# Performance work log

Measured on AMD Instinct MI355X. Metric: run time of the kernel, lower is better.

Reference implementation:

```python
import jax, jax.numpy as jnp
import numpy as np
from jax import lax

B_, NF, H, W = 2, 8, 32, 32
DIM = 384            # mamba_feat_dim = pT*pH*pW*hid_dim = 2*2*2*48
D_INNER = 192        # expand=0.5 -> int(0.5*384)
D_STATE = 16
D_CONV = 4
DT_RANK = 24         # ceil(DIM/16)
HIDDEN = 1536        # mlp_ratio=4
L = NF * H * W


def _ln(x, w, b):
    m = x.mean(-1, keepdims=True)
    v = ((x - m) ** 2).mean(-1, keepdims=True)
    return (x - m) * lax.rsqrt(v + 1e-5) * w + b


def _mamba(xn, in_proj_w, conv_w, conv_b, xproj_w, dt_w, dt_b, A_log, Dp, out_proj_w):
    # xn: [b, L, DIM]
    b = xn.shape[0]
    xz = jnp.einsum('bld,ed->ble', xn, in_proj_w)            # [b,L,2*di]
    xp, z = xz[..., :D_INNER], xz[..., D_INNER:]
    # causal depthwise conv along L (mamba_ssm pads left d_conv-1)
    xc = lax.conv_general_dilated(xp.swapaxes(1, 2), conv_w[:, None, :], (1,),
                                  [(D_CONV - 1, 0)],
                                  dimension_numbers=('NCH', 'OIH', 'NCH'),
                                  feature_group_count=D_INNER) + conv_b[None, :, None]
    xc = jax.nn.silu(xc).swapaxes(1, 2)                      # [b,L,di]
    dbl = jnp.einsum('bld,ed->ble', xc, xproj_w)             # [b,L,dt_rank+2*ds]
    dt = jax.nn.softplus(jnp.einsum('blr,dr->bld', dbl[..., :DT_RANK], dt_w) + dt_b)
    Bm = dbl[..., DT_RANK:DT_RANK + D_STATE]
    Cm = dbl[..., DT_RANK + D_STATE:]
    A = -jnp.exp(A_log)                                      # [di,ds]

    def step(h, inp):
        dt_t, B_t, C_t, x_t = inp                            # [b,di],[b,ds],[b,ds],[b,di]
        dA = jnp.exp(dt_t[..., None] * A)                    # [b,di,ds]
        h = dA * h + dt_t[..., None] * B_t[:, None, :] * x_t[..., None]
        return h, jnp.einsum('bds,bs->bd', h, C_t)

    h0 = jnp.zeros((b, D_INNER, D_STATE), xn.dtype)
    _, ys = lax.scan(step, h0, (dt.swapaxes(0, 1), Bm.swapaxes(0, 1),
                                Cm.swapaxes(0, 1), xc.swapaxes(0, 1)))
    y = ys.swapaxes(0, 1) + Dp * xc
    y = y * jax.nn.silu(z)
    return jnp.einsum('ble,de->bld', y, out_proj_w)


def _ssa(seqs, ssa_w):
    # sequence shuffle attention: grouped 1x1 conv over per-sequence pooled features
    pooled = jnp.stack([s.mean(1) for s in seqs], 1)          # [b,3,c]
    w = jnp.einsum('bsd,dts->btd', pooled, ssa_w)             # per-channel 3x3 mix
    aw = jax.nn.softmax(w, axis=1)                            # softmax over sequences
    st = jnp.stack(seqs, 0)                                   # [3,b,L,c]
    return jnp.einsum('btd,tbld->bld', aw, st)


def _mlp(x, fc1_w, fc1_b, dw_w, dw_b, fc2_w, fc2_b):
    b = x.shape[0]
    h1 = jnp.einsum('bld,ed->ble', x, fc1_w) + fc1_b          # [b,L,HIDDEN]
    hv = h1.swapaxes(1, 2).reshape(b, HIDDEN, NF, H, W)
    hv = lax.conv_general_dilated(hv, dw_w, (1, 1, 1), [(1, 1)] * 3,
                                  dimension_numbers=('NCDHW', 'OIDHW', 'NCDHW'),
                                  feature_group_count=HIDDEN) + dw_b[None, :, None, None, None]
    h1 = hv.reshape(b, HIDDEN, L).swapaxes(1, 2)
    h1 = jax.nn.gelu(h1, approximate=False)
    return jnp.einsum('ble,de->bld', h1, fc2_w) + fc2_b


def _forward(x, freq_x, ln1_w, ln1_b, in_proj_w, conv_w, conv_b, xproj_w, dt_w, dt_b,
             A_log, Dp, out_proj_w, ssa_w, ln2_w, ln2_b, fc1_w, fc1_b, dw_w, dw_b,
             fc2_w, fc2_b, hilbert_curve):
    b = x.shape[0]
    xc = x.transpose(0, 2, 1, 3, 4).reshape(b, DIM, L)        # [b,c,L]
    x_flat = xc[:, :, hilbert_curve].swapaxes(1, 2)           # hilbert gather -> [b,L,c]
    fc = freq_x.transpose(0, 2, 1, 3, 4).reshape(b, DIM, L)
    f_flat = fc[:, :, hilbert_curve].swapaxes(1, 2)
    normed = _ln(x_flat, ln1_w, ln1_b)
    mparams = (in_proj_w, conv_w, conv_b, xproj_w, dt_w, dt_b, A_log, Dp, out_proj_w)
    m_fwd = _mamba(normed, *mparams)
    m_rev = jnp.flip(_mamba(jnp.flip(normed, 1), *mparams), 1)
    mo = _ssa([m_fwd, m_rev, f_flat], ssa_w)
    xm = x_flat + mo
    xm = xm + _mlp(_ln(xm, ln2_w, ln2_b), fc1_w, fc1_b, dw_w, dw_b, fc2_w, fc2_b)
    outm = xm.swapaxes(1, 2)                                  # [b,c,L]
    inv = jnp.argsort(hilbert_curve)                          # inverse permutation (scatter)
    uns = outm[:, :, inv]
    return uns.reshape(b, DIM, NF, H, W).transpose(0, 2, 1, 3, 4)


def setup_inputs() -> dict:
    key = jax.random.key(0)
    ks = jax.random.split(key, 12)
    def n(i, shape, s=0.02):
        return jax.random.normal(ks[i], shape, jnp.float32) * s
    perm = jnp.asarray(np.random.default_rng(0).permutation(L), jnp.int32)
    return {
        'x': jax.random.normal(ks[0], (B_, NF, DIM, H, W), jnp.float32),
        'freq_x': jax.random.normal(ks[1], (B_, NF, DIM, H, W), jnp.float32),
        'hilbert_curve': perm,
        'ln1_w': jnp.ones((DIM,), jnp.float32), 'ln1_b': jnp.zeros((DIM,), jnp.float32),
        'in_proj_w': n(2, (2 * D_INNER, DIM)),
        'conv_w': n(3, (D_INNER, D_CONV), 0.1), 'conv_b': jnp.zeros((D_INNER,), jnp.float32),
        'xproj_w': n(4, (DT_RANK + 2 * D_STATE, D_INNER)),
        'dt_w': n(5, (D_INNER, DT_RANK), 0.1),
        'dt_b': jnp.full((D_INNER,), -4.6, jnp.float32),
        'A_log': jnp.log(jnp.tile(jnp.arange(1, D_STATE + 1, dtype=jnp.float32)[None, :], (D_INNER, 1))),
        'Dp': jnp.ones((D_INNER,), jnp.float32),
        'out_proj_w': n(6, (DIM, D_INNER)),
        'ssa_w': n(7, (DIM, 3, 3)),
        'ln2_w': jnp.ones((DIM,), jnp.float32), 'ln2_b': jnp.zeros((DIM,), jnp.float32),
        'fc1_w': n(8, (HIDDEN, DIM)), 'fc1_b': jnp.zeros((HIDDEN,), jnp.float32),
        'dw_w': n(9, (HIDDEN, 1, 3, 3, 3), 0.05), 'dw_b': jnp.zeros((HIDDEN,), jnp.float32),
        'fc2_w': n(10, (DIM, HIDDEN)), 'fc2_b': jnp.zeros((DIM,), jnp.float32),
    }


def reference(x, freq_x, hilbert_curve, ln1_w, ln1_b, in_proj_w, conv_w, conv_b,
              xproj_w, dt_w, dt_b, A_log, Dp, out_proj_w, ssa_w, ln2_w, ln2_b,
              fc1_w, fc1_b, dw_w, dw_b, fc2_w, fc2_b):
    return _forward(x, freq_x, ln1_w, ln1_b, in_proj_w, conv_w, conv_b, xproj_w,
                    dt_w, dt_b, A_log, Dp, out_proj_w, ssa_w, ln2_w, ln2_b,
                    fc1_w, fc1_b, dw_w, dw_b, fc2_w, fc2_b, hilbert_curve)
```

## Files before the change

kernel.cpp:

```cpp
#include <hip/hip_runtime.h>
#include <cmath>

#define B_N 2
#define NFR 8
#define HH 32
#define WW 32
#define LSEQ 8192
#define DIMD 384
#define DI 192
#define DST 16
#define DRK 24
#define HID 1536
#define MR (B_N*LSEQ)

#define NCH 256
#define CL  (LSEQ/NCH)
#define PSL 128

typedef __attribute__((ext_vector_type(8))) short  bf16x8;
typedef __attribute__((ext_vector_type(4))) float  f32x4;
typedef __attribute__((ext_vector_type(8))) unsigned short u16x8;

constexpr size_t SZ_BLD = (size_t)MR * DIMD;
constexpr size_t SZ_BLI = (size_t)MR * DI;
constexpr size_t SZ_DBL = (size_t)MR * 56;

constexpr size_t OFF_XFLAT = 0;
constexpr size_t OFF_FFLAT = OFF_XFLAT + SZ_BLD;
constexpr size_t OFF_XZ    = OFF_FFLAT + SZ_BLD;
constexpr size_t OFF_XCF   = OFF_XZ + SZ_BLD;
constexpr size_t OFF_XCR   = OFF_XCF + SZ_BLI;
constexpr size_t OFF_H1    = 0;
constexpr size_t OFF_PK    = 0;
constexpr size_t OFF_R2    = OFF_XCR + SZ_BLI;
constexpr size_t OFF_DBLF  = OFF_R2;
constexpr size_t OFF_DBLR  = OFF_DBLF + SZ_DBL;
constexpr size_t OFF_DTF   = OFF_DBLR + SZ_DBL;
constexpr size_t OFF_DTR   = OFF_DTF + SZ_BLI;
constexpr size_t OFF_GF    = OFF_DTR + SZ_BLI;
constexpr size_t OFF_GR    = OFF_GF + SZ_BLI;
constexpr size_t OFF_MF    = OFF_GR + SZ_BLI;
constexpr size_t OFF_MR_   = OFF_MF + SZ_BLD;
constexpr size_t OFF_H2    = OFF_R2;
constexpr size_t OFF_NORM  = OFF_MR_ + SZ_BLD;
constexpr size_t OFF_XM    = OFF_NORM + SZ_BLD;
constexpr size_t OFF_PART  = OFF_XM + SZ_BLD;
constexpr size_t OFF_AW    = OFF_PART + (size_t)6*PSL*384;
constexpr size_t OFF_INV   = OFF_AW + 2*3*384;
constexpr size_t OFF_WBF   = OFF_INV + 8192;
constexpr size_t WB_INP = 0;
constexpr size_t WB_OUT = WB_INP + 147456;
constexpr size_t WB_FC1 = WB_OUT + 73728;
constexpr size_t WB_FC2 = WB_FC1 + 589824;
constexpr size_t WB_TOT = WB_FC2 + 589824;
constexpr size_t SZ_CH   = (size_t)2*B_N*NCH*DI*16;
constexpr size_t OFF_CA  = OFF_NORM;
constexpr size_t OFF_CB  = OFF_CA + SZ_CH;
constexpr size_t OFF_CHS = OFF_CB + SZ_CH;
static_assert(OFF_CHS + SZ_CH <= OFF_PART, "scan summaries overflow");
static_assert(27*HID <= 6*PSL*384, "dwwT overflows part region");

__device__ __forceinline__ float siluf(float x){ return x / (1.f + expf(-x)); }
__device__ __forceinline__ float softplusf(float x){ return x > 20.f ? x : log1pf(expf(x)); }
__device__ __forceinline__ float geluf(float x){ return 0.5f * x * (1.f + erff(x * 0.70710678118f)); }
__device__ __forceinline__ unsigned short f2bf(float f){
    union { float f; unsigned int u; } v; v.f = f;
    unsigned int u = v.u + 0x7fffu + ((v.u >> 16) & 1u);
    return (unsigned short)(u >> 16);
}

#if __has_builtin(__builtin_amdgcn_global_load_lds)
#define HAVE_GLL 1
__device__ __forceinline__ void gload16(const void* g, void* l){
    __builtin_amdgcn_global_load_lds((const __attribute__((address_space(1))) void*)g,
                                     (__attribute__((address_space(3))) void*)l, 16, 0, 0);
}
#else
#define HAVE_GLL 0
#endif

__global__ __launch_bounds__(256)
void k_inv(const int* __restrict__ hc, int* __restrict__ inv)
{
    int l = blockIdx.x*256 + threadIdx.x;
    inv[hc[l]] = l;
}

__global__ __launch_bounds__(256)
void k_wcvt(const float* __restrict__ inpw, const float* __restrict__ outpw,
            const float* __restrict__ fc1w, const float* __restrict__ fc2w,
            unsigned short* __restrict__ wbf)
{
    int idx = blockIdx.x*256 + threadIdx.x;
    if (idx < 147456)                wbf[WB_INP + idx] = f2bf(inpw[idx]);
    else if (idx < 147456+73728)     wbf[WB_OUT + idx-147456] = f2bf(outpw[idx-147456]);
    else if (idx < 221184+589824)    wbf[WB_FC1 + idx-221184] = f2bf(fc1w[idx-221184]);
    else if (idx < 811008+589824)    wbf[WB_FC2 + idx-811008] = f2bf(fc2w[idx-811008]);
}

__global__ __launch_bounds__(256)
void k_wt(const float* __restrict__ dww, float* __restrict__ dwwT)
{
    int idx = blockIdx.x*256 + threadIdx.x;
    if (idx < 27*HID){
        int c = idx / 27, i = idx % 27;
        dwwT[i*HID + c] = dww[idx];
    }
}

__global__ __launch_bounds__(256)
void k_gather_ln(const float* __restrict__ x, const float* __restrict__ fx,
                 const int* __restrict__ inv, const float* __restrict__ lw,
                 const float* __restrict__ lb, float* __restrict__ x_flat,
                 float* __restrict__ f_flat, unsigned short* __restrict__ normed)
{
    __shared__ float tile[DIMD*33];
    int hw0 = blockIdx.x * 32;
    int nf  = blockIdx.y;
    int zz  = blockIdx.z;
    int b = zz >> 1, ph = zz & 1;
    int t   = threadIdx.x;
    int hwi = t & 31, dr = t >> 5;
    int w = t >> 6, lane = t & 63;
    const float* src = (ph ? fx : x) + ((size_t)(b*NFR+nf)*DIMD)*1024 + hw0;

    for (int d0 = 0; d0 < DIMD; d0 += 8){
        int d = d0 + dr;
        tile[d*33 + hwi] = src[(size_t)d*1024 + hwi];
    }
    __syncthreads();
    if (ph == 0){
        #pragma unroll
        for (int i = 0; i < 8; ++i){
            int r = w*8 + i;
            int l = inv[nf*1024 + hw0 + r];
            size_t rowo = (size_t)(b*LSEQ + l)*DIMD;
            float v[6]; float s = 0.f, s2 = 0.f;
            #pragma unroll
            for (int c = 0; c < 6; ++c){
                float a = tile[(c*64 + lane)*33 + r];
                v[c] = a; s += a; s2 += a*a;
            }
            #pragma unroll
            for (int o = 1; o < 64; o <<= 1){ s += __shfl_xor(s, o); s2 += __shfl_xor(s2, o); }
            float mean = s * (1.f/DIMD);
            float var  = s2 * (1.f/DIMD) - mean*mean;
            float rs = rsqrtf(var + 1e-5f);
            #pragma unroll
            for (int c = 0; c < 6; ++c){
                int d = c*64 + lane;
                x_flat[rowo + d] = v[c];
                normed[rowo + d] = f2bf((v[c]-mean)*rs*lw[d] + lb[d]);
            }
        }
    } else {
        #pragma unroll
        for (int i = 0; i < 8; ++i){
            int r = w*8 + i;
            int l = inv[nf*1024 + hw0 + r];
            size_t rowo = (size_t)(b*LSEQ + l)*DIMD;
            #pragma unroll
            for (int c = 0; c < 6; ++c)
                f_flat[rowo + c*64 + lane] = tile[(c*64 + lane)*33 + r];
        }
    }
}

__global__ __launch_bounds__(256)
void k_scatter(const float* __restrict__ outm, const float* __restrict__ pk,
               const int* __restrict__ inv, float* __restrict__ outp)
{
    __shared__ float tile[DIMD*33];
    int hw0 = blockIdx.x * 32;
    int nf  = blockIdx.y;
    int b   = blockIdx.z;
    int t   = threadIdx.x;
    int hwi = t & 31, dr = t >> 5;
    int w = t >> 6, lane = t & 63;
    #pragma unroll
    for (int i = 0; i < 8; ++i){
        int r = w*8 + i;
        int l = inv[nf*1024 + hw0 + r];
        size_t rowo = (size_t)(b*LSEQ + l)*DIMD;
        #pragma unroll
        for (int c = 0; c < 6; ++c){
            size_t o = rowo + c*64 + lane;
            tile[(c*64 + lane)*33 + r] = outm[o] + pk[o] + pk[SZ_BLD + o] + pk[2*SZ_BLD + o];
        }
    }
    __syncthreads();
    float* ob = outp + ((size_t)(b*NFR+nf)*DIMD)*1024 + hw0;
    for (int d0 = 0; d0 < DIMD; d0 += 8){
        int d = d0 + dr;
        ob[(size_t)d*1024 + hwi] = tile[d*33 + hwi];
    }
}

__global__ __launch_bounds__(128)
void k_ln(const float* __restrict__ in, const float* __restrict__ lw,
          const float* __restrict__ lb, unsigned short* __restrict__ out)
{
    size_t row = blockIdx.x;
    int t = threadIdx.x;
    float v[3]; float s = 0.f, s2 = 0.f;
    #pragma unroll
    for (int i = 0; i < 3; ++i){
        int d = t + i*128;
        float a = in[row*DIMD + d];
        v[i] = a; s += a; s2 += a*a;
    }
    #pragma unroll
    for (int o = 32; o > 0; o >>= 1){ s += __shfl_down(s, o); s2 += __shfl_down(s2, o); }
    __shared__ float sh[4];
    if ((t & 63) == 0){ sh[(t>>6)*2] = s; sh[(t>>6)*2+1] = s2; }
    __syncthreads();
    float S = sh[0] + sh[2], S2 = sh[1] + sh[3];
    float mean = S * (1.f/DIMD);
    float var  = S2 * (1.f/DIMD) - mean*mean;
    float r = rsqrtf(var + 1e-5f);
    #pragma unroll
    for (int i = 0; i < 3; ++i){
        int d = t + i*128;
        out[row*DIMD + d] = f2bf((v[i]-mean)*r*lw[d] + lb[d]);
    }
}

template<int EPI>
__global__ __launch_bounds__(256, 2)
void k_bgemm(const unsigned short* __restrict__ A, const unsigned short* __restrict__ Wb,
             const float* __restrict__ bias, const float* __restrict__ add,
             float* __restrict__ C, int N, int Kext, int Kstr)
{
    __shared__ unsigned short As[128*32];
    __shared__ unsigned short Bs[128*32];
    int tid  = threadIdx.x;
    int wid  = tid >> 6, lane = tid & 63;
    int row0 = blockIdx.x * 128, col0 = blockIdx.y * 128;
    int wr = wid >> 1, wc = wid & 1;
    int lr = lane & 15, lg = lane >> 4;

    f32x4 acc[4][4];
    #pragma unroll
    for (int m = 0; m < 4; ++m)
        #pragma unroll
        for (int n = 0; n < 4; ++n) acc[m][n] = (f32x4){0.f,0.f,0.f,0.f};

    int s0 = wid*2048 + lane*16;
    int r0 = s0 >> 6, k0i = (s0 & 63) >> 1;
    int s1 = s0 + 1024;
    int r1 = s1 >> 6, k1i = (s1 & 63) >> 1;
    const unsigned short* Ag0 = A  + (size_t)(row0 + r0)*Kstr + k0i;
    const unsigned short* Ag1 = A  + (size_t)(row0 + r1)*Kstr + k1i;
    const unsigned short* Bg0 = Wb + (size_t)(col0 + r0)*Kstr + k0i;
    const unsigned short* Bg1 = Wb + (size_t)(col0 + r1)*Kstr + k1i;

    const unsigned short* Ab = &As[(wr*64 + lr)*32 + lg*8];
    const unsigned short* Bb = &Bs[(wc*64 + lr)*32 + lg*8];

    for (int k0 = 0; k0 < Kext; k0 += 32){
        if (k0) __syncthreads();
#if HAVE_GLL
        gload16(Ag0, (char*)As + wid*2048);
        gload16(Ag1, (char*)As + wid*2048 + 1024);
        gload16(Bg0, (char*)Bs + wid*2048);
        gload16(Bg1, (char*)Bs + wid*2048 + 1024);
#else
        *(u16x8*)((char*)As + s0) = *(const u16x8*)Ag0;
        *(u16x8*)((char*)As + s1) = *(const u16x8*)Ag1;
        *(u16x8*)((char*)Bs + s0) = *(const u16x8*)Bg0;
        *(u16x8*)((char*)Bs + s1) = *(const u16x8*)Bg1;
#endif
        Ag0 += 32; Ag1 += 32; Bg0 += 32; Bg1 += 32;
        __syncthreads();
        bf16x8 af[4], bfr[4];
        #pragma unroll
        for (int m = 0; m < 4; ++m) af[m]  = *(const bf16x8*)(Ab + m*512);
        #pragma unroll
        for (int n = 0; n < 4; ++n) bfr[n] = *(const bf16x8*)(Bb + n*512);
        #pragma unroll
        for (int m = 0; m < 4; ++m)
            #pragma unroll
            for (int n = 0; n < 4; ++n)
                acc[m][n] = __builtin_amdgcn_mfma_f32_16x16x32_bf16(af[m], bfr[n], acc[m][n], 0, 0, 0);
    }

    #pragma unroll
    for (int m = 0; m < 4; ++m){
        #pragma unroll
        for (int r = 0; r < 4; ++r){
            int row = row0 + wr*64 + m*16 + lg*4 + r;
            #pragma unroll
            for (int n = 0; n < 4; ++n){
                int col = col0 + wc*64 + n*16 + lr;
                float v = acc[m][n][r];
                if (EPI >= 1) v += bias[col];
                if (EPI == 2) v += add[(size_t)row*N + col];
                C[(size_t)row*N + col] = v;
            }
        }
    }
}

__global__ __launch_bounds__(256, 2)
void k_bgemm_sk(const unsigned short* __restrict__ A, const unsigned short* __restrict__ Wb,
                const float* __restrict__ bias, const float* __restrict__ add,
                float* __restrict__ C0, float* __restrict__ PK, int N, int Kq, int Kstr)
{
    __shared__ unsigned short As[128*32];
    __shared__ unsigned short Bs[128*32];
    int tid  = threadIdx.x;
    int wid  = tid >> 6, lane = tid & 63;
    int row0 = blockIdx.x * 128, col0 = blockIdx.y * 128;
    int z = blockIdx.z;
    int kbeg = z * Kq;
    int wr = wid >> 1, wc = wid & 1;
    int lr = lane & 15, lg = lane >> 4;

    f32x4 acc[4][4];
    #pragma unroll
    for (int m = 0; m < 4; ++m)
        #pragma unroll
        for (int n = 0; n < 4; ++n) acc[m][n] = (f32x4){0.f,0.f,0.f,0.f};

    int s0 = wid*2048 + lane*16;
    int r0 = s0 >> 6, k0i = (s0 & 63) >> 1;
    int s1 = s0 + 1024;
    int r1 = s1 >> 6, k1i = (s1 & 63) >> 1;
    const unsigned short* Ag0 = A  + (size_t)(row0 + r0)*Kstr + kbeg + k0i;
    const unsigned short* Ag1 = A  + (size_t)(row0 + r1)*Kstr + kbeg + k1i;
    const unsigned short* Bg0 = Wb + (size_t)(col0 + r0)*Kstr + kbeg + k0i;
    const unsigned short* Bg1 = Wb + (size_t)(col0 + r1)*Kstr + kbeg + k1i;

    const unsigned short* Ab = &As[(wr*64 + lr)*32 + lg*8];
    const unsigned short* Bb = &Bs[(wc*64 + lr)*32 + lg*8];

    for (int k0 = 0; k0 < Kq; k0 += 32){
        if (k0) __syncthreads();
#if HAVE_GLL
        gload16(Ag0, (char*)As + wid*2048);
        gload16(Ag1, (char*)As + wid*2048 + 1024);
        gload16(Bg0, (char*)Bs + wid*2048);
        gload16(Bg1, (char*)Bs + wid*2048 + 1024);
#else
        *(u16x8*)((char*)As + s0) = *(const u16x8*)Ag0;
        *(u16x8*)((char*)As + s1) = *(const u16x8*)Ag1;
        *(u16x8*)((char*)Bs + s0) = *(const u16x8*)Bg0;
        *(u16x8*)((char*)Bs + s1) = *(const u16x8*)Bg1;
#endif
        Ag0 += 32; Ag1 += 32; Bg0 += 32; Bg1 += 32;
        __syncthreads();
        bf16x8 af[4], bfr[4];
        #pragma unroll
        for (int m = 0; m < 4; ++m) af[m]  = *(const bf16x8*)(Ab + m*512);
        #pragma unroll
        for (int n = 0; n < 4; ++n) bfr[n] = *(const bf16x8*)(Bb + n*512);
        #pragma unroll
        for (int m = 0; m < 4; ++m)
            #pragma unroll
            for (int n = 0; n < 4; ++n)
                acc[m][n] = __builtin_amdgcn_mfma_f32_16x16x32_bf16(af[m], bfr[n], acc[m][n], 0, 0, 0);
    }

    float* Cdst = (z == 0) ? C0 : (PK + (size_t)(z-1)*SZ_BLD);
    #pragma unroll
    for (int m = 0; m < 4; ++m){
        #pragma unroll
        for (int r = 0; r < 4; ++r){
            int row = row0 + wr*64 + m*16 + lg*4 + r;
            #pragma unroll
            for (int n = 0; n < 4; ++n){
                int col = col0 + wc*64 + n*16 + lr;
                float v = acc[m][n][r];
                if (z == 0) v += bias[col] + add[(size_t)row*N + col];
                Cdst[(size_t)row*N + col] = v;
            }
        }
    }
}

__global__ __launch_bounds__(256)
void k_conv(const float* __restrict__ xz, const float* __restrict__ cw,
            const float* __restrict__ cb, float* __restrict__ xcf, float* __restrict__ xcr)
{
    const int TL = 64;
    int b = blockIdx.y;
    int l0 = blockIdx.x * TL;
    __shared__ float sx[TL+6][DI];
    for (int idx = threadIdx.x; idx < (TL+6)*DI; idx += 256){
        int r = idx / DI, c = idx % DI;
        int l = l0 + r - 3;
        float v = 0.f;
        if (l >= 0 && l < LSEQ) v = xz[((size_t)b*LSEQ + l)*DIMD + c];
        sx[r][c] = v;
    }
    __syncthreads();
    for (int idx = threadIdx.x; idx < TL*DI; idx += 256){
        int r = idx / DI, c = idx % DI;
        float w0 = cw[c*4+0], w1 = cw[c*4+1], w2 = cw[c*4+2], w3 = cw[c*4+3];
        float bi = cb[c];
        size_t orow = ((size_t)b*LSEQ + l0 + r)*DI + c;
        float af = bi + sx[r][c]*w0 + sx[r+1][c]*w1 + sx[r+2][c]*w2 + sx[r+3][c]*w3;
        xcf[orow] = siluf(af);
        float ar = bi + sx[r+3][c]*w3 + sx[r+4][c]*w2 + sx[r+5][c]*w1 + sx[r+6][c]*w0;
        xcr[orow] = siluf(ar);
    }
}

__global__ __launch_bounds__(256)
void k_dbl(const float* __restrict__ xc_f, const float* __restrict__ xc_r,
           const float* __restrict__ xpw,
           float* __restrict__ dbl_f, float* __restrict__ dbl_r)
{
    const float* xc  = blockIdx.y ? xc_r  : xc_f;
    float*       dbl = blockIdx.y ? dbl_r : dbl_f;
    __shared__ float sw[56*196];
    for (int i = threadIdx.x; i < 56*DI; i += 256){
        int n = i / DI, k = i % DI;
        sw[n*196 + k] = xpw[i];
    }
    __syncthreads();
    int lane = threadIdx.x & 63;
    int wid  = threadIdx.x >> 6;
    if (lane >= 56) return;
    const float* wrow = &sw[lane*196];
    #pragma unroll
    for (int g = 0; g < 2; ++g){
        int row0 = blockIdx.x*64 + g*32 + wid*8;
        const float* xr = xc + (size_t)row0*DI;
        float acc[8];
        #pragma unroll
        for (int r = 0; r < 8; ++r) acc[r] = 0.f;
        for (int k = 0; k < DI; k += 4){
            float4 w4 = *(const float4*)&wrow[k];
            #pragma unroll
            for (int r = 0; r < 8; ++r){
                float4 x4 = *(const float4*)&xr[(size_t)r*DI + k];
                acc[r] += x4.x*w4.x + x4.y*w4.y + x4.z*w4.z + x4.w*w4.w;
            }
        }
        #pragma unroll
        for (int r = 0; r < 8; ++r)
            dbl[(size_t)(row0 + r)*56 + lane] = acc[r];
    }
}

__global__ __launch_bounds__(192)
void k_dt(const float* __restrict__ dbl_f, const float* __restrict__ dbl_r,
          const float* __restrict__ dtw, const float* __restrict__ dtb,
          float* __restrict__ dt_f, float* __restrict__ dt_r)
{
    const float* dbl = blockIdx.y ? dbl_r : dbl_f;
    float*       dt  = blockIdx.y ? dt_r  : dt_f;
    int row0 = blockIdx.x * 8;
    int d = threadIdx.x;
    __shared__ float sd[8][24];
    {
        int lr = threadIdx.x / 24, lc = threadIdx.x % 24;
        sd[lr][lc] = dbl[(size_t)(row0 + lr)*56 + lc];
    }
    __syncthreads();
    float wreg[24];
    #pragma unroll
    for (int r = 0; r < DRK; ++r) wreg[r] = dtw[d*DRK + r];
    float bias = dtb[d];
    #pragma unroll
    for (int rr = 0; rr < 8; ++rr){
        float acc = bias;
        #pragma unroll
        for (int r = 0; r < DRK; ++r) acc += sd[rr][r] * wreg[r];
        dt[(size_t)(row0 + rr)*DI + d] = softplusf(acc);
    }
}

__global__ __launch_bounds__(384)
void k_scan_p1(const float* __restrict__ dt_f, const float* __restrict__ dt_r,
               const float* __restrict__ dbl_f, const float* __restrict__ dbl_r,
               const float* __restrict__ xc_f, const float* __restrict__ xc_r,
               const float* __restrict__ A_log,
               float* __restrict__ CA, float* __restrict__ CB)
{
    int ch = blockIdx.x, b = blockIdx.y, dir = blockIdx.z;
    const float* dt  = dir ? dt_r  : dt_f;
    const float* dbl = dir ? dbl_r : dbl_f;
    const float* xc  = dir ? xc_r  : xc_f;
    int t = threadIdx.x;
    int d = t >> 1, sh = (t & 1) * 8;
    float A2[8];
    #pragma unroll
    for (int s = 0; s < 8; ++s) A2[s] = -expf(A_log[d*DST + sh + s]) * 1.44269504f;
    float hB[8];
    #pragma unroll
    for (int s = 0; s < 8; ++s) hB[s] = 0.f;
    float sumdt = 0.f;
    __shared__ float sdt[16][192], sxc[16][192], sB[16][16];
    for (int t0 = 0; t0 < CL/16; ++t0){
        __syncthreads();
        #pragma unroll
        for (int q = 0; q < 2; ++q){
            int idx = t + q*384;
            int j = idx / 48, c4 = (idx % 48)*4;
            int lidx = ch*CL + t0*16 + j;
            int lld = dir ? (LSEQ-1-lidx) : lidx;
            size_t rowbl = (size_t)b*LSEQ + lld;
            *(float4*)&sdt[j][c4] = *(const float4*)&dt[rowbl*DI + c4];
            *(float4*)&sxc[j][c4] = *(const float4*)&xc[rowbl*DI + c4];
        }
        if (t < 256){
            int j = t >> 4, c = t & 15;
            int lidx = ch*CL + t0*16 + j;
            int lld = dir ? (LSEQ-1-lidx) : lidx;
            sB[j][c] = dbl[((size_t)b*LSEQ + lld)*56 + 24 + c];
        }
        __syncthreads();
        #pragma unroll 4
        for (int j = 0; j < 16; ++j){
            float dtv = sdt[j][d];
            float c0  = dtv * sxc[j][d];
            sumdt += dtv;
            #pragma unroll
            for (int s = 0; s < 8; ++s){
                float da = exp2f(dtv * A2[s]);
                hB[s] = da*hB[s] + c0*sB[j][sh + s];
            }
        }
    }
    size_t o = (((size_t)(dir*B_N + b)*NCH + ch)*DI + d)*16 + sh;
    #pragma unroll
    for (int s = 0; s < 8; ++s){
        CA[o + s] = exp2f(sumdt * A2[s]);
        CB[o + s] = hB[s];
    }
}

__global__ __launch_bounds__(256)
void k_scan_p2(const float* __restrict__ CA, const float* __restrict__ CB,
               float* __restrict__ CH)
{
    int b = blockIdx.y, dir = blockIdx.z;
    int t = blockIdx.x*256 + threadIdx.x;
    size_t base = ((size_t)(dir*B_N + b)*NCH)*(DI*16) + t;
    float h = 0.f;
    for (int c = 0; c < NCH; ++c){
        size_t o = base + (size_t)c*(DI*16);
        CH[o] = h;
        h = CA[o]*h + CB[o];
    }
}

__global__ __launch_bounds__(384)
void k_scan_p3(const float* __restrict__ dt_f, const float* __restrict__ dt_r,
               const float* __restrict__ dbl_f, const float* __restrict__ dbl_r,
               const float* __restrict__ xc_f, const float* __restrict__ xc_r,
               const float* __restrict__ xz, const float* __restrict__ A_log,
               const float* __restrict__ Dp, const float* __restrict__ CH,
               unsigned short* __restrict__ g_f, unsigned short* __restrict__ g_r)
{
    int ch = blockIdx.x, b = blockIdx.y, dir = blockIdx.z;
    const float* dt  = dir ? dt_r  : dt_f;
    const float* dbl = dir ? dbl_r : dbl_f;
    const float* xc  = dir ? xc_r  : xc_f;
    unsigned short* g = dir ? g_r : g_f;
    int t = threadIdx.x;
    int d = t >> 1, sh = (t & 1) * 8;
    float A2[8];
    #pragma unroll
    for (int s = 0; s < 8; ++s) A2[s] = -expf(A_log[d*DST + sh + s]) * 1.44269504f;
    float Dpd = Dp[d];
    float h[8];
    size_t so = (((size_t)(dir*B_N + b)*NCH + ch)*DI + d)*16 + sh;
    #pragma unroll
    for (int s = 0; s < 8; ++s) h[s] = CH[so + s];
    __shared__ float sdt[16][192], sxc[16][192], szv[16][192], sBC[16][32];
    int lld0 = dir ? (LSEQ-1 - ch*CL) : (ch*CL);
    long gstep = dir ? -(long)DI : (long)DI;
    unsigned short* gp = g + ((size_t)b*LSEQ + lld0)*DI + d;
    for (int t0 = 0; t0 < CL/16; ++t0){
        __syncthreads();
        #pragma unroll
        for (int q = 0; q < 2; ++q){
            int idx = t + q*384;
            int j = idx / 48, c4 = (idx % 48)*4;
            int lidx = ch*CL + t0*16 + j;
            int lld = dir ? (LSEQ-1-lidx) : lidx;
            size_t rowbl = (size_t)b*LSEQ + lld;
            *(float4*)&sdt[j][c4] = *(const float4*)&dt[rowbl*DI + c4];
            *(float4*)&sxc[j][c4] = *(const float4*)&xc[rowbl*DI + c4];
            *(float4*)&szv[j][c4] = *(const float4*)&xz[rowbl*DIMD + DI + c4];
        }
        for (int idx = t; idx < 512; idx += 384){
            int j = idx >> 5, c = idx & 31;
            int lidx = ch*CL + t0*16 + j;
            int lld = dir ? (LSEQ-1-lidx) : lidx;
            sBC[j][c] = dbl[((size_t)b*LSEQ + lld)*56 + 24 + c];
        }
        __syncthreads();
        #pragma unroll 4
        for (int j = 0; j < 16; ++j){
            float dtv = sdt[j][d];
            float xv  = sxc[j][d];
            float c0  = dtv * xv;
            float y = 0.f;
            #pragma unroll
            for (int s = 0; s < 8; ++s){
                float da = exp2f(dtv * A2[s]);
                h[s] = da*h[s] + c0*sBC[j][sh + s];
                y += h[s]*sBC[j][16 + sh + s];
            }
            y += __shfl_xor(y, 1);
            if ((t & 1) == 0){
                float zv = szv[j][d];
                *gp = f2bf((y + Dpd*xv) * siluf(zv));
            }
            gp += gstep;
        }
    }
}

__global__ __launch_bounds__(384)
void k_pool(const float* __restrict__ m_f, const float* __restrict__ m_r,
            const float* __restrict__ f_flat, float* __restrict__ partial)
{
    int bt = blockIdx.x;
    int sl = blockIdx.y;
    int b = bt / 3, t = bt % 3;
    const float* src = (t == 0) ? m_f : (t == 1) ? m_r : f_flat;
    src += (size_t)b*LSEQ*DIMD + (size_t)sl*(LSEQ/PSL)*DIMD;
    int d = threadIdx.x;
    float sum = 0.f;
    #pragma unroll 8
    for (int l = 0; l < LSEQ/PSL; ++l) sum += src[(size_t)l*DIMD + d];
    partial[((size_t)bt*PSL + sl)*DIMD + d] = sum;
}

__global__ __launch_bounds__(384)
void k_ssa(const float* __restrict__ partial, const float* __restrict__ ssaw,
           float* __restrict__ aw)
{
    int b = blockIdx.x;
    int d = threadIdx.x;
    float pooled[3];
    #pragma unroll
    for (int t = 0; t < 3; ++t){
        float sum = 0.f;
        for (int sl = 0; sl < PSL; ++sl) sum += partial[((size_t)(b*3+t)*PSL + sl)*DIMD + d];
        pooled[t] = sum * (1.f/LSEQ);
    }
    float wv[3];
    #pragma unroll
    for (int t = 0; t < 3; ++t)
        wv[t] = pooled[0]*ssaw[d*9 + t*3 + 0] + pooled[1]*ssaw[d*9 + t*3 + 1] + pooled[2]*ssaw[d*9 + t*3 + 2];
    float mx = fmaxf(wv[0], fmaxf(wv[1], wv[2]));
    float e0 = expf(wv[0]-mx), e1 = expf(wv[1]-mx), e2 = expf(wv[2]-mx);
    float inv_ = 1.f / (e0+e1+e2);
    aw[(size_t)(b*3+0)*DIMD + d] = e0*inv_;
    aw[(size_t)(b*3+1)*DIMD + d] = e1*inv_;
    aw[(size_t)(b*3+2)*DIMD + d] = e2*inv_;
}

__global__ __launch_bounds__(256)
void k_xm(const float* __restrict__ x_flat, const float* __restrict__ m_f,
          const float* __restrict__ m_r, const float* __restrict__ f_flat,
          const float* __restrict__ aw, float* __restrict__ xm)
{
    size_t idx = (size_t)blockIdx.x*256 + threadIdx.x;
    int d = (int)(idx % DIMD);
    size_t row = idx / DIMD;
    int b = (int)(row >> 13);
    float a0 = aw[(size_t)(b*3+0)*DIMD + d];
    float a1 = aw[(size_t)(b*3+1)*DIMD + d];
    float a2 = aw[(size_t)(b*3+2)*DIMD + d];
    xm[idx] = x_flat[idx] + a0*m_f[idx] + a1*m_r[idx] + a2*f_flat[idx];
}

__global__ __launch_bounds__(256)
void k_dwconv(const float* __restrict__ h1, const float* __restrict__ dwwT,
              const float* __restrict__ dwb, unsigned short* __restrict__ h2)
{
    int c = blockIdx.x*256 + threadIdx.x;
    int hy = blockIdx.y;
    int h = hy >> 1, w0 = (hy & 1) * 16;
    int bnf = blockIdx.z; int b = bnf >> 3, nf = bnf & 7;
    float acc[16];
    float bias = dwb[c];
    #pragma unroll
    for (int i = 0; i < 16; ++i) acc[i] = bias;
    const float* basep = h1 + (size_t)b*LSEQ*HID + c;
    #pragma unroll
    for (int dn = 0; dn < 3; ++dn){
        int pn = nf + dn - 1;
        if (pn < 0 || pn >= NFR) continue;
        float wt9[9];
        #pragma unroll
        for (int i = 0; i < 9; ++i) wt9[i] = dwwT[(size_t)(dn*9 + i)*HID + c];
        #pragma unroll
        for (int dh = 0; dh < 3; ++dh){
            int ph = h + dh - 1;
            if (ph < 0 || ph >= HH) continue;
            const float* row = basep + ((size_t)pn*1024 + (size_t)ph*32)*HID;
            float w_a = (w0 > 0) ? row[(size_t)(w0-1)*HID] : 0.f;
            float w_b = row[(size_t)w0*HID];
            float q0 = wt9[dh*3+0], q1 = wt9[dh*3+1], q2 = wt9[dh*3+2];
            #pragma unroll
            for (int xw = 0; xw < 16; ++xw){
                int wn = w0 + xw + 1;
                float w_c = (wn < WW) ? row[(size_t)wn*HID] : 0.f;
                acc[xw] += w_a*q0 + w_b*q1 + w_c*q2;
                w_a = w_b; w_b = w_c;
            }
        }
    }
    unsigned short* orow = h2 + ((size_t)b*LSEQ + nf*1024 + h*32 + w0)*HID + c;
    #pragma unroll
    for (int xw = 0; xw < 16; ++xw)
        orow[(size_t)xw*HID] = f2bf(geluf(acc[xw]));
}

extern "C" void kernel_launch(void* const* d_in, const int* in_sizes, int n_in,
                              void* d_out, int out_size, void* d_ws, size_t ws_size,
                              hipStream_t stream)
{
    const float* x     = (const float*)d_in[0];
    const float* fx    = (const float*)d_in[1];
    const int*   hc    = (const int*)  d_in[2];
    const float* ln1w  = (const float*)d_in[3];
    const float* ln1b  = (const float*)d_in[4];
    const float* inpw  = (const float*)d_in[5];
    const float* convw = (const float*)d_in[6];
    const float* convb = (const float*)d_in[7];
    const float* xpw   = (const float*)d_in[8];
    const float* dtw   = (const float*)d_in[9];
    const float* dtb   = (const float*)d_in[10];
    const float* alog  = (const float*)d_in[11];
    const float* dp    = (const float*)d_in[12];
    const float* outpw = (const float*)d_in[13];
    const float* ssaw  = (const float*)d_in[14];
    const float* ln2w  = (const float*)d_in[15];
    const float* ln2b  = (const float*)d_in[16];
    const float* fc1w  = (const float*)d_in[17];
    const float* fc1b  = (const float*)d_in[18];
    const float* dww   = (const float*)d_in[19];
    const float* dwb   = (const float*)d_in[20];
    const float* fc2w  = (const float*)d_in[21];
    const float* fc2b  = (const float*)d_in[22];

    float* ws = (float*)d_ws;
    float* x_flat = ws + OFF_XFLAT;
    float* f_flat = ws + OFF_FFLAT;
    float* xz     = ws + OFF_XZ;
    float* xc_f   = ws + OFF_XCF;
    float* xc_r   = ws + OFF_XCR;
    float* dbl_f  = ws + OFF_DBLF;
    float* dbl_r  = ws + OFF_DBLR;
    float* dt_f   = ws + OFF_DTF;
    float* dt_r   = ws + OFF_DTR;
    float* m_f    = ws + OFF_MF;
    float* m_r    = ws + OFF_MR_;
    float* h1     = ws + OFF_H1;
    float* pkbuf  = ws + OFF_PK;
    float* xm     = ws + OFF_XM;
    float* part   = ws + OFF_PART;
    float* dwwT   = ws + OFF_PART;
    float* aw     = ws + OFF_AW;
    float* cA     = ws + OFF_CA;
    float* cB     = ws + OFF_CB;
    float* cH     = ws + OFF_CHS;
    float* outm   = ws + OFF_NORM;
    int*   inv    = (int*)(ws + OFF_INV);
    unsigned short* wbf    = (unsigned short*)(ws + OFF_WBF);
    unsigned short* inpw_b = wbf + WB_INP;
    unsigned short* outpw_b= wbf + WB_OUT;
    unsigned short* fc1w_b = wbf + WB_FC1;
    unsigned short* fc2w_b = wbf + WB_FC2;
    unsigned short* nrm_bf = (unsigned short*)(ws + OFF_NORM);
    unsigned short* gf_bf  = (unsigned short*)(ws + OFF_GF);
    unsigned short* gr_bf  = (unsigned short*)(ws + OFF_GR);
    unsigned short* h2_bf  = (unsigned short*)(ws + OFF_H2);
    float* outp   = (float*)d_out;

    k_inv<<<LSEQ/256, 256, 0, stream>>>(hc, inv);
    k_wcvt<<<(int)((WB_TOT + 255)/256), 256, 0, stream>>>(inpw, outpw, fc1w, fc2w, wbf);
    k_gather_ln<<<dim3(32, NFR, B_N*2), 256, 0, stream>>>(x, fx, inv, ln1w, ln1b, x_flat, f_flat, nrm_bf);
    k_bgemm<0><<<dim3(128,3), 256, 0, stream>>>(nrm_bf, inpw_b, nullptr, nullptr, xz, DIMD, DIMD, DIMD);
    k_conv<<<dim3(LSEQ/64, B_N), 256, 0, stream>>>(xz, convw, convb, xc_f, xc_r);
    k_dbl<<<dim3(MR/64, 2), 256, 0, stream>>>(xc_f, xc_r, xpw, dbl_f, dbl_r);
    k_dt<<<dim3(MR/8, 2), 192, 0, stream>>>(dbl_f, dbl_r, dtw, dtb, dt_f, dt_r);
    k_scan_p1<<<dim3(NCH, B_N, 2), 384, 0, stream>>>(dt_f, dt_r, dbl_f, dbl_r, xc_f, xc_r, alog, cA, cB);
    k_scan_p2<<<dim3(DI*16/256, B_N, 2), 256, 0, stream>>>(cA, cB, cH);
    k_scan_p3<<<dim3(NCH, B_N, 2), 384, 0, stream>>>(dt_f, dt_r, dbl_f, dbl_r, xc_f, xc_r, xz, alog, dp, cH, gf_bf, gr_bf);
    k_bgemm<0><<<dim3(128,3), 256, 0, stream>>>(gf_bf, outpw_b, nullptr, nullptr, m_f, DIMD, DI, DI);
    k_bgemm<0><<<dim3(128,3), 256, 0, stream>>>(gr_bf, outpw_b, nullptr, nullptr, m_r, DIMD, DI, DI);
    k_pool<<<dim3(6,PSL), 384, 0, stream>>>(m_f, m_r, f_flat, part);
    k_ssa<<<B_N, 384, 0, stream>>>(part, ssaw, aw);
    k_wt<<<(27*HID + 255)/256, 256, 0, stream>>>(dww, dwwT);
    k_xm<<<(unsigned)(SZ_BLD/256), 256, 0, stream>>>(x_flat, m_f, m_r, f_flat, aw, xm);
    k_ln<<<MR, 128, 0, stream>>>(xm, ln2w, ln2b, nrm_bf);
    k_bgemm<1><<<dim3(128,12), 256, 0, stream>>>(nrm_bf, fc1w_b, fc1b, nullptr, h1, HID, DIMD, DIMD);
    k_dwconv<<<dim3(6,64,16), 256, 0, stream>>>(h1, dwwT, dwb, h2_bf);
    k_bgemm_sk<<<dim3(128,3,4), 256, 0, stream>>>(h2_bf, fc2w_b, fc2b, xm, outm, pkbuf, DIMD, HID/4, HID);
    k_scatter<<<dim3(32, NFR, B_N), 256, 0, stream>>>(outm, pkbuf, inv, outp);
}
```

Baseline: 532.4 us.

## Fuse residual mix into LayerNorm, vectorize depthwise conv, use tanh GELU

Merges the elementwise residual/attention-weight mix kernel into the second LayerNorm, which removes one launch and a full re-read of xm. The depthwise 3D conv now handles two channels per thread with float2 loads and packed bf16 stores, halving its grid. The exact erf GELU is replaced by the tanh approximation built on a fast exp, a small numerical deviation from the reference erf GELU.

Result: slower. 544.8 us (+2.3%).

```diff
diff --git a/kernel.cpp b/kernel.cpp
--- a/kernel.cpp
+++ b/kernel.cpp
@@ -62,7 +62,12 @@
 
 __device__ __forceinline__ float siluf(float x){ return x / (1.f + expf(-x)); }
 __device__ __forceinline__ float softplusf(float x){ return x > 20.f ? x : log1pf(expf(x)); }
-__device__ __forceinline__ float geluf(float x){ return 0.5f * x * (1.f + erff(x * 0.70710678118f)); }
+__device__ __forceinline__ float gelut(float x){
+    float z = 0.7978845608f*(x + 0.044715f*x*x*x);
+    float e = __expf(2.f*z);
+    float t = 1.f - 2.f/(e + 1.f);
+    return 0.5f*x*(1.f + t);
+}
 __device__ __forceinline__ unsigned short f2bf(float f){
     union { float f; unsigned int u; } v; v.f = f;
     unsigned int u = v.u + 0x7fffu + ((v.u >> 16) & 1u);
@@ -197,17 +202,26 @@
 }
 
 __global__ __launch_bounds__(128)
-void k_ln(const float* __restrict__ in, const float* __restrict__ lw,
-          const float* __restrict__ lb, unsigned short* __restrict__ out)
+void k_xm_ln(const float* __restrict__ x_flat, const float* __restrict__ m_f,
+             const float* __restrict__ m_r, const float* __restrict__ f_flat,
+             const float* __restrict__ aw, const float* __restrict__ lw,
+             const float* __restrict__ lb, float* __restrict__ xm,
+             unsigned short* __restrict__ out)
 {
     size_t row = blockIdx.x;
+    int b = (int)(row >> 13);
     int t = threadIdx.x;
     float v[3]; float s = 0.f, s2 = 0.f;
     #pragma unroll
     for (int i = 0; i < 3; ++i){
         int d = t + i*128;
-        float a = in[row*DIMD + d];
-        v[i] = a; s += a; s2 += a*a;
+        size_t o = row*DIMD + d;
+        float a0 = aw[(size_t)(b*3+0)*DIMD + d];
+        float a1 = aw[(size_t)(b*3+1)*DIMD + d];
+        float a2 = aw[(size_t)(b*3+2)*DIMD + d];
+        float val = x_flat[o] + a0*m_f[o] + a1*m_r[o] + a2*f_flat[o];
+        xm[o] = val;
+        v[i] = val; s += val; s2 += val*val;
     }
     #pragma unroll
     for (int o = 32; o > 0; o >>= 1){ s += __shfl_down(s, o); s2 += __shfl_down(s2, o); }
@@ -658,30 +672,17 @@
 }
 
 __global__ __launch_bounds__(256)
-void k_xm(const float* __restrict__ x_flat, const float* __restrict__ m_f,
-          const float* __restrict__ m_r, const float* __restrict__ f_flat,
-          const float* __restrict__ aw, float* __restrict__ xm)
-{
-    size_t idx = (size_t)blockIdx.x*256 + threadIdx.x;
-    int d = (int)(idx % DIMD);
-    size_t row = idx / DIMD;
-    int b = (int)(row >> 13);
-    float a0 = aw[(size_t)(b*3+0)*DIMD + d];
-    float a1 = aw[(size_t)(b*3+1)*DIMD + d];
-    float a2 = aw[(size_t)(b*3+2)*DIMD + d];
-    xm[idx] = x_flat[idx] + a0*m_f[idx] + a1*m_r[idx] + a2*f_flat[idx];
-}
-
-__global__ __launch_bounds__(256)
 void k_dwconv(const float* __restrict__ h1, const float* __restrict__ dwwT,
               const float* __restrict__ dwb, unsigned short* __restrict__ h2)
 {
-    int c = blockIdx.x*256 + threadIdx.x;
+    int cp = blockIdx.x*256 + threadIdx.x;
+    int c  = cp*2;
     int hy = blockIdx.y;
     int h = hy >> 1, w0 = (hy & 1) * 16;
     int bnf = blockIdx.z; int b = bnf >> 3, nf = bnf & 7;
-    float acc[16];
-    float bias = dwb[c];
+    const float2 z2 = {0.f, 0.f};
+    float2 acc[16];
+    float2 bias = *(const float2*)&dwb[c];
     #pragma unroll
     for (int i = 0; i < 16; ++i) acc[i] = bias;
     const float* basep = h1 + (size_t)b*LSEQ*HID + c;
@@ -689,30 +690,38 @@
     for (int dn = 0; dn < 3; ++dn){
         int pn = nf + dn - 1;
         if (pn < 0 || pn >= NFR) continue;
-        float wt9[9];
-        #pragma unroll
-        for (int i = 0; i < 9; ++i) wt9[i] = dwwT[(size_t)(dn*9 + i)*HID + c];
+        float2 wt9[9];
+        #pragma unroll
+        for (int i = 0; i < 9; ++i) wt9[i] = *(const float2*)&dwwT[(size_t)(dn*9 + i)*HID + c];
         #pragma unroll
         for (int dh = 0; dh < 3; ++dh){
             int ph = h + dh - 1;
             if (ph < 0 || ph >= HH) continue;
             const float* row = basep + ((size_t)pn*1024 + (size_t)ph*32)*HID;
-            float w_a = (w0 > 0) ? row[(size_t)(w0-1)*HID] : 0.f;
-            float w_b = row[(size_t)w0*HID];
-            float q0 = wt9[dh*3+0], q1 = wt9[dh*3+1], q2 = wt9[dh*3+2];
+            float2 w_a = (w0 > 0) ? *(const float2*)&row[(size_t)(w0-1)*HID] : z2;
+            const float* pc = row + (size_t)w0*HID;
+            float2 w_b = *(const float2*)pc;
+            pc += HID;
+            float2 q0 = wt9[dh*3+0], q1 = wt9[dh*3+1], q2 = wt9[dh*3+2];
             #pragma unroll
             for (int xw = 0; xw < 16; ++xw){
                 int wn = w0 + xw + 1;
-                float w_c = (wn < WW) ? row[(size_t)wn*HID] : 0.f;
-                acc[xw] += w_a*q0 + w_b*q1 + w_c*q2;
+                float2 w_c = (wn < WW) ? *(const float2*)pc : z2;
+                pc += HID;
+                acc[xw].x += w_a.x*q0.x + w_b.x*q1.x + w_c.x*q2.x;
+                acc[xw].y += w_a.y*q0.y + w_b.y*q1.y + w_c.y*q2.y;
                 w_a = w_b; w_b = w_c;
             }
         }
     }
     unsigned short* orow = h2 + ((size_t)b*LSEQ + nf*1024 + h*32 + w0)*HID + c;
     #pragma unroll
-    for (int xw = 0; xw < 16; ++xw)
-        orow[(size_t)xw*HID] = f2bf(geluf(acc[xw]));
+    for (int xw = 0; xw < 16; ++xw){
+        union { unsigned short u[2]; unsigned int v; } pk;
+        pk.u[0] = f2bf(gelut(acc[xw].x));
+        pk.u[1] = f2bf(gelut(acc[xw].y));
+        *(unsigned int*)(orow + (size_t)xw*HID) = pk.v;
+    }
 }
 
 extern "C" void kernel_launch(void* const* d_in, const int* in_sizes, int n_in,
@@ -792,10 +801,9 @@
     k_pool<<<dim3(6,PSL), 384, 0, stream>>>(m_f, m_r, f_flat, part);
     k_ssa<<<B_N, 384, 0, stream>>>(part, ssaw, aw);
     k_wt<<<(27*HID + 255)/256, 256, 0, stream>>>(dww, dwwT);
-    k_xm<<<(unsigned)(SZ_BLD/256), 256, 0, stream>>>(x_flat, m_f, m_r, f_flat, aw, xm);
-    k_ln<<<MR, 128, 0, stream>>>(xm, ln2w, ln2b, nrm_bf);
+    k_xm_ln<<<MR, 128, 0, stream>>>(x_flat, m_f, m_r, f_flat, aw, ln2w, ln2b, xm, nrm_bf);
     k_bgemm<1><<<dim3(128,12), 256, 0, stream>>>(nrm_bf, fc1w_b, fc1b, nullptr, h1, HID, DIMD, DIMD);
-    k_dwconv<<<dim3(6,64,16), 256, 0, stream>>>(h1, dwwT, dwb, h2_bf);
+    k_dwconv<<<dim3(3,64,16), 256, 0, stream>>>(h1, dwwT, dwb, h2_bf);
     k_bgemm_sk<<<dim3(128,3,4), 256, 0, stream>>>(h2_bf, fc2w_b, fc2b, xm, outm, pkbuf, DIMD, HID/4, HID);
     k_scatter<<<dim3(32, NFR, B_N), 256, 0, stream>>>(outm, pkbuf, inv, outp);
 }
```
